# Kernel optimization log

Hardware: AMD Instinct MI355X
Metric: run time of the kernel (lower is better)

## Reference

```python
import jax, jax.numpy as jnp
import numpy as np

H = 1024
W = 1024
K = 3  # kernel_size
N = H * W
TWO_PI = 2.0 * np.pi


def setup_inputs() -> dict:
    key = jax.random.key(0)
    ks = jax.random.split(key, 8)
    latent = jax.random.normal(ks[0], (H, W, 4), dtype=jnp.float32)
    raw_pos = jax.random.randint(ks[1], (N, 2), 0, W, dtype=jnp.int32)
    control = jax.random.normal(ks[2], (N, 2), dtype=jnp.float32)
    def lin(k, fan_in, fan_out):
        bound = 1.0 / np.sqrt(fan_in)
        return jax.random.uniform(k, (fan_in, fan_out), jnp.float32, -bound, bound)
    W1 = lin(ks[3], 108, 64); b1 = jnp.zeros((64,), jnp.float32)
    W2 = lin(ks[4], 64, 128); b2 = jnp.zeros((128,), jnp.float32)
    W3 = lin(ks[5], 128, 64); b3 = jnp.zeros((64,), jnp.float32)
    W4 = lin(ks[6], 64, 4);   b4 = jnp.zeros((4,), jnp.float32)
    return dict(latent=latent, raw_pos=raw_pos, control=control,
                W1=W1, b1=b1, W2=W2, b2=b2, W3=W3, b3=b3, W4=W4, b4=b4)


def reference(latent, raw_pos, control, W1, b1, W2, b2, W3, b3, W4, b4):
    # --- kernel expand: 3x3 neighbor coords, clamped at edges ---
    offs = jnp.arange(-(K // 2), K // 2 + 1)
    xo, yo = jnp.meshgrid(offs, offs, indexing='ij')  # [K,K]
    ex = jnp.clip(raw_pos[:, 0:1] + xo.ravel()[None, :], 0, W - 1)  # [N, K*K]
    ey = jnp.clip(raw_pos[:, 1:2] + yo.ravel()[None, :], 0, H - 1)  # [N, K*K]

    # --- neighbor gather via computed linear indices ---
    lin_idx = ey * W + ex                                   # [N, K*K]
    latent_values = latent.reshape(-1, latent.shape[-1])[lin_idx]  # [N, K*K, 4]

    # --- positional encodings (num_encodings=6, non-exponential) ---
    xf = ex.astype(jnp.float32) / W                         # already clamped
    yf = ey.astype(jnp.float32) / H
    pos_enc = jnp.stack([
        xf, yf,
        jnp.sin(TWO_PI * 1 * xf), jnp.sin(TWO_PI * 1 * yf),
        jnp.sin(TWO_PI * 2 * xf), jnp.sin(TWO_PI * 2 * yf),
    ], axis=-1)                                             # [N, K*K, 6]

    # --- control broadcast across kernel positions ---
    ctrl = jnp.broadcast_to(control[:, None, :], (control.shape[0], K * K, control.shape[-1]))

    patches = jnp.concatenate([latent_values, pos_enc, ctrl], axis=-1)  # [N, K*K, 12]
    x = patches.reshape(patches.shape[0], -1)               # [N, 108]

    # --- tiny MLP: Linear+GELU(exact) x3, Linear+Sigmoid ---
    gelu = lambda t: jax.nn.gelu(t, approximate=False)
    x = gelu(x @ W1 + b1)
    x = gelu(x @ W2 + b2)
    x = gelu(x @ W3 + b3)
    return jax.nn.sigmoid(x @ W4 + b4)                      # [N, 4]
```

## Files before the change

kernel.cpp:

```cpp
#include <hip/hip_runtime.h>
#include <hip/hip_bf16.h>
#include <math.h>

#define IMG 1024
#define NPIXTOT (IMG * IMG)
#define TWO_PI_F 6.28318530717958647692f

typedef __attribute__((ext_vector_type(8))) short short8;
typedef __attribute__((ext_vector_type(4))) float f32x4;
typedef unsigned int uint;
typedef unsigned short ushort;

#define A1_OFF 0
#define A2_OFF 8192
#define A3_OFF 16384
#define A4_OFF 24576
#define WTOT   25600
#define GLUT_N   3072
#define GLUT_OFF WTOT
#define SLUT_OFF (GLUT_OFF + GLUT_N)
#define SLUT_N   2048
#define WSTOT    (SLUT_OFF + SLUT_N)

#define LATBF_BYTEOFF 65536

__device__ __forceinline__ ushort f2bf(float f) {
    uint u = __float_as_uint(f);
    u += 0x7fffu + ((u >> 16) & 1u);
    return (ushort)(u >> 16);
}
__device__ __forceinline__ uint pack2(float a, float b) {
    float2 t; t.x = a; t.y = b;
    __hip_bfloat162 h = __float22bfloat162_rn(t);
    union { __hip_bfloat162 h; uint u; } cv; cv.h = h;
    return cv.u;
}
__device__ __forceinline__ float sig_fast(float x) {
    return __builtin_amdgcn_rcpf(1.0f + __expf(-x));
}

__device__ __forceinline__ uint gelu2(float x0, float x1, const ushort* __restrict__ g) {
    union { uint u; ushort h[2]; } w;
    w.h[0] = g[(int)__builtin_amdgcn_fmed3f(fmaf(x0, 256.0f, 1536.5f), 0.0f, 3071.0f)];
    w.h[1] = g[(int)__builtin_amdgcn_fmed3f(fmaf(x1, 256.0f, 1536.5f), 0.0f, 3071.0f)];
    return w.u;
}

__device__ __forceinline__ int permM(int k) {
    return (2 * (k >> 5) + ((k >> 2) & 1)) * 16 + 4 * ((k >> 3) & 3) + (k & 3);
}

__device__ __forceinline__ int2 nbc(int2 rp, int n) {
    const int dxi = (n * 86) >> 8;
    int2 c;
    c.x = min(max(rp.x + dxi - 1, 0), IMG - 1);
    c.y = min(max(rp.y + (n - 3 * dxi) - 1, 0), IMG - 1);
    return c;
}

__global__ void prep_weights(const float* __restrict__ W1, const float* __restrict__ b1,
                             const float* __restrict__ W2, const float* __restrict__ W3,
                             const float* __restrict__ W4, ushort* __restrict__ ws) {
    int e = blockIdx.x * 256 + threadIdx.x;
    if (e >= WSTOT) return;
    float v;
    if (e < A2_OFF) {
        int i = e & 7, lo = (e >> 3) & 15, hi = (e >> 7) & 3, kst = e >> 9;
        int ks = kst & 3;
        int m = (kst >> 2) * 16 + lo;
        int korig;
        if (ks < 2)       korig = 12 * (2 * hi + ks) + i;
        else if (ks == 2) korig = 12 * (2 * hi + (i >> 2)) + 8 + (i & 3);
        else {
            if (hi == 0)      korig = 96 + i;
            else if (hi == 1) korig = (i < 4) ? 104 + i : (i == 4 ? 108 : 999);
            else              korig = 999;
        }
        v = (korig < 108) ? W1[korig * 64 + m] : (korig == 108 ? b1[m] : 0.0f);
    } else if (e < A3_OFF) {
        int r = e - A2_OFF, i = r & 7, lo = (r >> 3) & 15, hi = (r >> 7) & 3, kst = r >> 9;
        int m = (kst >> 1) * 16 + lo, k = (kst & 1) * 32 + hi * 8 + i;
        v = W2[permM(k) * 128 + m];
    } else if (e < A4_OFF) {
        int r = e - A3_OFF, i = r & 7, lo = (r >> 3) & 15, hi = (r >> 7) & 3, kst = r >> 9;
        int m = (kst >> 2) * 16 + lo, k = (kst & 3) * 32 + hi * 8 + i;
        v = W3[permM(k) * 64 + m];
    } else if (e < GLUT_OFF) {
        int r = e - A4_OFF, i = r & 7, lo = (r >> 3) & 15, hi = (r >> 7) & 3, ks = (r >> 9) & 1;
        int k = ks * 32 + hi * 8 + i;
        v = (lo < 4) ? W4[permM(k) * 4 + lo] : 0.0f;
    } else if (e < SLUT_OFF) {
        const float x = (float)(e - GLUT_OFF - 1536) * (1.0f / 256.0f);
        v = 0.5f * x * (1.0f + erff(x * 0.70710678118654752440f));
    } else {
        const int j = e - SLUT_OFF;
        const float a = (float)(j >> 1) * (1.0f / 1024.0f);
        v = sinf(((j & 1) ? 2.0f : 1.0f) * TWO_PI_F * a);
    }
    ws[e] = f2bf(v);
}

__global__ void prep_latent(const float* __restrict__ lat, ushort* __restrict__ dst) {
    const int i = blockIdx.x * 256 + threadIdx.x;
    if (i >= NPIXTOT) return;
    const float4 v = ((const float4*)lat)[i];
    union { ushort h[4]; uint2 u; } o;
    o.h[0] = f2bf(v.x); o.h[1] = f2bf(v.y); o.h[2] = f2bf(v.z); o.h[3] = f2bf(v.w);
    ((uint2*)dst)[i] = o.u;
}

template<int KS, int KSN, bool HASB>
__device__ __forceinline__ void mlayer_reg(const short8 (&bin)[2][KS], short8 (&bout)[2][KSN],
                                           const ushort* wA,
                                           const float* __restrict__ bias,
                                           const ushort* gl, int lo, int hi) {
    #pragma unroll
    for (int kn = 0; kn < KSN; ++kn) {
        f32x4 acc[2][2];
        #pragma unroll
        for (int b = 0; b < 2; ++b) {
            const int nt = 2 * kn + b;
            if (HASB) {
                const float4 bv = *(const float4*)&bias[nt * 16 + hi * 4];
                acc[b][0] = f32x4{bv.x, bv.y, bv.z, bv.w};
            } else {
                acc[b][0] = f32x4{0.f, 0.f, 0.f, 0.f};
            }
            acc[b][1] = acc[b][0];
            #pragma unroll
            for (int ks = 0; ks < KS; ++ks) {
                const short8 a = *(const short8*)&wA[(nt * KS + ks) * 512 + (hi * 16 + lo) * 8];
                acc[b][0] = __builtin_amdgcn_mfma_f32_16x16x32_bf16(a, bin[0][ks], acc[b][0], 0, 0, 0);
                acc[b][1] = __builtin_amdgcn_mfma_f32_16x16x32_bf16(a, bin[1][ks], acc[b][1], 0, 0, 0);
            }
        }
        #pragma unroll
        for (int pt = 0; pt < 2; ++pt) {
            union { short8 s; uint u[4]; } o;
            o.u[0] = gelu2(acc[0][pt][0], acc[0][pt][1], gl);
            o.u[1] = gelu2(acc[0][pt][2], acc[0][pt][3], gl);
            o.u[2] = gelu2(acc[1][pt][0], acc[1][pt][1], gl);
            o.u[3] = gelu2(acc[1][pt][2], acc[1][pt][3], gl);
            bout[pt][kn] = o.s;
        }
    }
}

template<bool BF>
__global__ __launch_bounds__(512, 2) void vfx_mfma(
    const float* __restrict__ latent, const uint2* __restrict__ latbf,
    const int* __restrict__ raw_pos, const float* __restrict__ control,
    const ushort* __restrict__ wsrc,
    const float* __restrict__ b2, const float* __restrict__ b3,
    const float* __restrict__ b4, float* __restrict__ out)
{
    __shared__ ushort wl[WSTOT];
    const int tid = threadIdx.x;
    const int wave = tid >> 6, lane = tid & 63;
    const int lo = lane & 15, hi = lane >> 4;
    const int pixbase = blockIdx.x * 256 + wave * 32;

    {
        const uint4* src = (const uint4*)wsrc;
        uint4* dst = (uint4*)wl;
        #pragma unroll
        for (int it = 0; it < 8; ++it) {
            const int i = tid + it * 512;
            if (i < 3840) dst[i] = src[i];
        }
    }

    const int g0 = pixbase + lo, g1 = pixbase + 16 + lo;
    const int2 rp0 = ((const int2*)raw_pos)[g0];
    const int2 rp1 = ((const int2*)raw_pos)[g1];
    const float2 cf0 = ((const float2*)control)[g0];
    const float2 cf1 = ((const float2*)control)[g1];

    const int na = 2 * hi, nbb = 2 * hi + 1;
    const int2 cA0 = nbc(rp0, na), cB0 = nbc(rp0, nbb);
    const int2 cA1 = nbc(rp1, na), cB1 = nbc(rp1, nbb);
    const int2 c80 = nbc(rp0, 8),  c81 = nbc(rp1, 8);

    uint2 lA0, lB0, lA1, lB1, l80, l81;
    if (BF) {
        lA0 = latbf[(cA0.y << 10) + cA0.x]; lB0 = latbf[(cB0.y << 10) + cB0.x];
        lA1 = latbf[(cA1.y << 10) + cA1.x]; lB1 = latbf[(cB1.y << 10) + cB1.x];
        if (hi == 0) { l80 = latbf[(c80.y << 10) + c80.x]; l81 = latbf[(c81.y << 10) + c81.x]; }
    } else {
        const float4* lf = (const float4*)latent;
        float4 a;
        a = lf[(cA0.y << 10) + cA0.x]; lA0 = make_uint2(pack2(a.x, a.y), pack2(a.z, a.w));
        a = lf[(cB0.y << 10) + cB0.x]; lB0 = make_uint2(pack2(a.x, a.y), pack2(a.z, a.w));
        a = lf[(cA1.y << 10) + cA1.x]; lA1 = make_uint2(pack2(a.x, a.y), pack2(a.z, a.w));
        a = lf[(cB1.y << 10) + cB1.x]; lB1 = make_uint2(pack2(a.x, a.y), pack2(a.z, a.w));
        if (hi == 0) {
            a = lf[(c80.y << 10) + c80.x]; l80 = make_uint2(pack2(a.x, a.y), pack2(a.z, a.w));
            a = lf[(c81.y << 10) + c81.x]; l81 = make_uint2(pack2(a.x, a.y), pack2(a.z, a.w));
        }
    }

    __syncthreads();
    const ushort* glut = wl + GLUT_OFF;
    const uint*   slut = (const uint*)(wl + SLUT_OFF);

    short8 bX[2][4];
    {
        auto mk = [&](int2 c, uint2 lat, uint& s2u) -> short8 {
            const uint sx = slut[c.x], sy = slut[c.y];
            s2u = (sx >> 16) | (sy & 0xffff0000u);
            union { short8 s; uint u[4]; } o;
            o.u[0] = lat.x; o.u[1] = lat.y;
            o.u[2] = pack2((float)c.x * (1.0f / IMG), (float)c.y * (1.0f / IMG));
            o.u[3] = (sx & 0xffffu) | (sy << 16);
            return o.s;
        };
        uint s2a0, s2b0, s2a1, s2b1;
        bX[0][0] = mk(cA0, lA0, s2a0);
        bX[0][1] = mk(cB0, lB0, s2b0);
        bX[1][0] = mk(cA1, lA1, s2a1);
        bX[1][1] = mk(cB1, lB1, s2b1);
        const uint upc0 = pack2(cf0.x, cf0.y), upc1 = pack2(cf1.x, cf1.y);
        union { short8 s; uint u[4]; } t;
        t.u[0] = s2a0; t.u[1] = upc0; t.u[2] = s2b0; t.u[3] = upc0; bX[0][2] = t.s;
        t.u[0] = s2a1; t.u[1] = upc1; t.u[2] = s2b1; t.u[3] = upc1; bX[1][2] = t.s;
        if (hi == 0) {
            uint d0, d1;
            bX[0][3] = mk(c80, l80, d0);
            bX[1][3] = mk(c81, l81, d1);
        } else if (hi == 1) {
            union { short8 s; uint u[4]; } o;
            o.u[0] = (slut[c80.x] >> 16) | (slut[c80.y] & 0xffff0000u);
            o.u[1] = upc0; o.u[2] = 0x3f80u; o.u[3] = 0u;
            bX[0][3] = o.s;
            o.u[0] = (slut[c81.x] >> 16) | (slut[c81.y] & 0xffff0000u);
            o.u[1] = upc1;
            bX[1][3] = o.s;
        } else {
            union { short8 s; uint u[4]; } z;
            z.u[0] = 0u; z.u[1] = 0u; z.u[2] = 0u; z.u[3] = 0u;
            bX[0][3] = z.s; bX[1][3] = z.s;
        }
    }

    short8 h1[2][2], h2[2][4], h3[2][2];
    mlayer_reg<4, 2, false>(bX, h1, wl + A1_OFF, nullptr, glut, lo, hi);
    mlayer_reg<2, 4, true >(h1, h2, wl + A2_OFF, b2, glut, lo, hi);
    mlayer_reg<4, 2, true >(h2, h3, wl + A3_OFF, b3, glut, lo, hi);

    {
        float4 bv = {0.f, 0.f, 0.f, 0.f};
        if (hi == 0) bv = *(const float4*)b4;
        f32x4 acc0 = {bv.x, bv.y, bv.z, bv.w};
        f32x4 acc1 = acc0;
        #pragma unroll
        for (int ks = 0; ks < 2; ++ks) {
            const short8 a = *(const short8*)&wl[A4_OFF + (ks * 512) + (hi * 16 + lo) * 8];
            acc0 = __builtin_amdgcn_mfma_f32_16x16x32_bf16(a, h3[0][ks], acc0, 0, 0, 0);
            acc1 = __builtin_amdgcn_mfma_f32_16x16x32_bf16(a, h3[1][ks], acc1, 0, 0, 0);
        }
        if (hi == 0) {
            float4 o;
            o.x = sig_fast(acc0[0]); o.y = sig_fast(acc0[1]);
            o.z = sig_fast(acc0[2]); o.w = sig_fast(acc0[3]);
            *(float4*)&out[(pixbase + lo) * 4] = o;
            o.x = sig_fast(acc1[0]); o.y = sig_fast(acc1[1]);
            o.z = sig_fast(acc1[2]); o.w = sig_fast(acc1[3]);
            *(float4*)&out[(pixbase + 16 + lo) * 4] = o;
        }
    }
}

extern "C" void kernel_launch(void* const* d_in, const int* in_sizes, int n_in,
                              void* d_out, int out_size, void* d_ws, size_t ws_size,
                              hipStream_t stream) {
    const float* latent  = (const float*)d_in[0];
    const int*   raw_pos = (const int*)  d_in[1];
    const float* control = (const float*)d_in[2];
    const float* W1 = (const float*)d_in[3];
    const float* b1 = (const float*)d_in[4];
    const float* W2 = (const float*)d_in[5];
    const float* b2 = (const float*)d_in[6];
    const float* W3 = (const float*)d_in[7];
    const float* b3 = (const float*)d_in[8];
    const float* W4 = (const float*)d_in[9];
    const float* b4 = (const float*)d_in[10];
    float* out = (float*)d_out;
    ushort* ws = (ushort*)d_ws;

    prep_weights<<<dim3((WSTOT + 255) / 256), dim3(256), 0, stream>>>(W1, b1, W2, W3, W4, ws);

    const size_t need = (size_t)LATBF_BYTEOFF + (size_t)NPIXTOT * 8;
    const bool use_bf = ws_size >= need;
    dim3 grid(NPIXTOT / 256);

    if (use_bf) {
        ushort* latbf = (ushort*)((char*)d_ws + LATBF_BYTEOFF);
        prep_latent<<<dim3(NPIXTOT / 256), dim3(256), 0, stream>>>(latent, latbf);
        vfx_mfma<true><<<grid, dim3(512), 0, stream>>>(
            latent, (const uint2*)latbf, raw_pos, control, ws, b2, b3, b4, out);
    } else {
        vfx_mfma<false><<<grid, dim3(512), 0, stream>>>(
            latent, nullptr, raw_pos, control, ws, b2, b3, b4, out);
    }
}
```

Baseline: 101.5 us.

## Double-buffer MLP weight loads from LDS and raise occupancy target

Each MLP layer now prefetches the next output tile's weight fragments from shared memory into a register double buffer while the current tile's MFMAs run. This is meant to hide LDS latency behind matrix work. The launch bounds hint also goes from 2 to 4 blocks per CU, which squeezes registers while the prefetch buffers need more of them, so spills are a risk. The __restrict__ on the gelu LUT pointer is dropped.

```diff
diff --git a/kernel.cpp b/kernel.cpp
--- a/kernel.cpp
+++ b/kernel.cpp
@@ -39,7 +39,7 @@
     return __builtin_amdgcn_rcpf(1.0f + __expf(-x));
 }
 
-__device__ __forceinline__ uint gelu2(float x0, float x1, const ushort* __restrict__ g) {
+__device__ __forceinline__ uint gelu2(float x0, float x1, const ushort* g) {
     union { uint u; ushort h[2]; } w;
     w.h[0] = g[(int)__builtin_amdgcn_fmed3f(fmaf(x0, 256.0f, 1536.5f), 0.0f, 3071.0f)];
     w.h[1] = g[(int)__builtin_amdgcn_fmed3f(fmaf(x1, 256.0f, 1536.5f), 0.0f, 3071.0f)];
@@ -110,18 +110,29 @@
 }
 
 template<int KS, int KSN, bool HASB>
-__device__ __forceinline__ void mlayer_reg(const short8 (&bin)[2][KS], short8 (&bout)[2][KSN],
-                                           const ushort* wA,
-                                           const float* __restrict__ bias,
-                                           const ushort* gl, int lo, int hi) {
+__device__ __forceinline__ void mlayer_pf(const short8 (&bin)[2][KS], short8 (&bout)[2][KSN],
+                                          const ushort* wA,
+                                          const float* __restrict__ bias,
+                                          const ushort* gl, int lo, int hi) {
+    const int lane8 = (hi * 16 + lo) * 8;
+    short8 a[2][2 * KS];
+    #pragma unroll
+    for (int t = 0; t < 2 * KS; ++t)
+        a[0][t] = *(const short8*)&wA[t * 512 + lane8];
+
     #pragma unroll
     for (int kn = 0; kn < KSN; ++kn) {
+        if (kn + 1 < KSN) {
+            #pragma unroll
+            for (int t = 0; t < 2 * KS; ++t)
+                a[(kn + 1) & 1][t] =
+                    *(const short8*)&wA[((kn + 1) * 2 * KS + t) * 512 + lane8];
+        }
         f32x4 acc[2][2];
         #pragma unroll
         for (int b = 0; b < 2; ++b) {
-            const int nt = 2 * kn + b;
             if (HASB) {
-                const float4 bv = *(const float4*)&bias[nt * 16 + hi * 4];
+                const float4 bv = *(const float4*)&bias[(2 * kn + b) * 16 + hi * 4];
                 acc[b][0] = f32x4{bv.x, bv.y, bv.z, bv.w};
             } else {
                 acc[b][0] = f32x4{0.f, 0.f, 0.f, 0.f};
@@ -129,9 +140,9 @@
             acc[b][1] = acc[b][0];
             #pragma unroll
             for (int ks = 0; ks < KS; ++ks) {
-                const short8 a = *(const short8*)&wA[(nt * KS + ks) * 512 + (hi * 16 + lo) * 8];
-                acc[b][0] = __builtin_amdgcn_mfma_f32_16x16x32_bf16(a, bin[0][ks], acc[b][0], 0, 0, 0);
-                acc[b][1] = __builtin_amdgcn_mfma_f32_16x16x32_bf16(a, bin[1][ks], acc[b][1], 0, 0, 0);
+                const short8 av = a[kn & 1][b * KS + ks];
+                acc[b][0] = __builtin_amdgcn_mfma_f32_16x16x32_bf16(av, bin[0][ks], acc[b][0], 0, 0, 0);
+                acc[b][1] = __builtin_amdgcn_mfma_f32_16x16x32_bf16(av, bin[1][ks], acc[b][1], 0, 0, 0);
             }
         }
         #pragma unroll
@@ -147,7 +158,7 @@
 }
 
 template<bool BF>
-__global__ __launch_bounds__(512, 2) void vfx_mfma(
+__global__ __launch_bounds__(512, 4) void vfx_mfma(
     const float* __restrict__ latent, const uint2* __restrict__ latbf,
     const int* __restrict__ raw_pos, const float* __restrict__ control,
     const ushort* __restrict__ wsrc,
@@ -243,9 +254,9 @@
     }
 
     short8 h1[2][2], h2[2][4], h3[2][2];
-    mlayer_reg<4, 2, false>(bX, h1, wl + A1_OFF, nullptr, glut, lo, hi);
-    mlayer_reg<2, 4, true >(h1, h2, wl + A2_OFF, b2, glut, lo, hi);
-    mlayer_reg<4, 2, true >(h2, h3, wl + A3_OFF, b3, glut, lo, hi);
+    mlayer_pf<4, 2, false>(bX, h1, wl + A1_OFF, nullptr, glut, lo, hi);
+    mlayer_pf<2, 4, true >(h1, h2, wl + A2_OFF, b2, glut, lo, hi);
+    mlayer_pf<4, 2, true >(h2, h3, wl + A3_OFF, b3, glut, lo, hi);
 
     {
         float4 bv = {0.f, 0.f, 0.f, 0.f};
```

Measured after the change: 101.2 us. No clear change (-0.3%).
